# Kernel tuning notes

Hardware: AMD Instinct MI355X
Metric: run time of the kernel (lower is better)

## Reference

```python
import jax, jax.numpy as jnp
import numpy as np

HEADS = 8
DIM_HEAD = 64
WINDOW = 128
PERSIST = 4
EPS = 1.1920929e-07  # torch nn.RMSNorm default eps = finfo(fp32).eps


def _rope_freqs(n, d, dtype):
    inv_freq = 1.0 / (10000.0 ** (jnp.arange(0, d, 2, dtype=jnp.float32) / d))
    freqs = jnp.arange(n, dtype=jnp.float32)[:, None] * inv_freq[None, :]  # [n, d/2]
    freqs = jnp.repeat(freqs, 2, axis=-1)  # interleaved repeat -> [n, d]
    return jnp.cos(freqs).astype(dtype), jnp.sin(freqs).astype(dtype)


def _rotate_half(x):
    # interleaved pairs (x0,x1),(x2,x3)... -> (-x1,x0),(-x3,x2)...
    x = x.reshape(*x.shape[:-1], -1, 2)
    x1, x2 = x[..., 0], x[..., 1]
    return jnp.stack((-x2, x1), axis=-1).reshape(*x.shape[:-2], -1)


def setup_inputs() -> dict:
    key = jax.random.key(0)
    k1, k2, k3 = jax.random.split(key, 3)
    B, N, D = 1, 4096, 1024
    dim_inner = HEADS * DIM_HEAD  # 512
    return {
        "seq": jax.random.normal(k1, (B, N, D), dtype=jnp.float32),
        "g": jnp.ones((D,), dtype=jnp.float32),
        "w_qkv": jax.random.normal(k2, (D, 3 * dim_inner), dtype=jnp.float32) * 0.02,
        "w_out": jax.random.normal(k3, (dim_inner, D), dtype=jnp.float32) * 0.02,
    }


def reference(seq, g, w_qkv, w_out):
    B, N, D = seq.shape
    H, Dh = HEADS, DIM_HEAD

    # RMSNorm
    x = seq * jax.lax.rsqrt(jnp.mean(seq * seq, axis=-1, keepdims=True) + EPS) * g

    # QKV projection -> [B, H, N, Dh]
    qkv = x @ w_qkv
    q, k, v = jnp.split(qkv, 3, axis=-1)
    to_heads = lambda t: t.reshape(B, N, H, Dh).transpose(0, 2, 1, 3)
    q, k, v = map(to_heads, (q, k, v))

    # rotary embeddings (same positions for q and k)
    cos, sin = _rope_freqs(N, Dh, q.dtype)
    q = q * cos + _rotate_half(q) * sin
    k = k * cos + _rotate_half(k) * sin

    # causal & (persist | sliding-window) mask
    idx = jnp.arange(N)
    dist = idx[:, None] - idx[None, :]
    mask = (dist >= 0) & ((idx[None, :] < PERSIST) | (dist <= WINDOW))  # [N, N]

    scale = Dh ** -0.5
    scores = jnp.einsum("bhid,bhjd->bhij", q, k) * scale
    neg = -jnp.finfo(scores.dtype).max
    scores = jnp.where(mask[None, None], scores, neg)
    attn = jax.nn.softmax(scores, axis=-1)
    out = jnp.einsum("bhij,bhjd->bhid", attn, v)

    out = out.transpose(0, 2, 1, 3).reshape(B, N, H * Dh)
    return out @ w_out
```

## Files before the change

### kernel.cpp

```cpp
#include <hip/hip_runtime.h>
#include <hip/hip_bf16.h>
#include <math.h>

#define SEQ    4096
#define DMODEL 1024
#define NHEADS 8
#define DH     64
#define DINNER 512
#define NQKV   1536
#define WINDOW 128
#define PERSIST 4
#define EPS 1.1920929e-07f

typedef unsigned short u16;
typedef unsigned int   u32;
typedef __bf16  bf16_8 __attribute__((ext_vector_type(8)));
typedef float   f32x4  __attribute__((ext_vector_type(4)));

__device__ __forceinline__ u16 f2b(float f) {
    union { float f; u32 i; } v; v.f = f;
    u32 i = v.i;
    u32 r = (i + 0x7fffu + ((i >> 16) & 1u)) >> 16;
    return (u16)r;
}

#define GLD16(gp, lp) __builtin_amdgcn_global_load_lds( \
    (const __attribute__((address_space(1))) void*)(gp), \
    (__attribute__((address_space(3))) void*)(lp), 16, 0, 0)

__device__ __forceinline__ void transpose_tile(const float* __restrict__ src,
                                               u16* __restrict__ dst,
                                               int K, int N, int bn, int bk,
                                               u16 (*t)[65], int tid) {
    int r = tid >> 4, c4 = (tid & 15) * 4;
    #pragma unroll
    for (int it = 0; it < 4; it++) {
        int row = r + it * 16;
        float4 v = *(const float4*)(src + (size_t)(bk + row) * N + bn + c4);
        t[row][c4 + 0] = f2b(v.x);
        t[row][c4 + 1] = f2b(v.y);
        t[row][c4 + 2] = f2b(v.z);
        t[row][c4 + 3] = f2b(v.w);
    }
    __syncthreads();
    #pragma unroll
    for (int it = 0; it < 4; it++) {
        int n = r + it * 16;
        u16* d = dst + (size_t)(bn + n) * K + bk + c4;
        uint2 o;
        o.x = (u32)t[c4 + 0][n] | ((u32)t[c4 + 1][n] << 16);
        o.y = (u32)t[c4 + 2][n] | ((u32)t[c4 + 3][n] << 16);
        *(uint2*)d = o;
    }
}

__global__ __launch_bounds__(256) void prep_kernel(const float* __restrict__ wqkv,
                                                   const float* __restrict__ wout,
                                                   const float* __restrict__ seq,
                                                   const float* __restrict__ g,
                                                   u16* __restrict__ wqkv_bt,
                                                   u16* __restrict__ wout_bt,
                                                   u16* __restrict__ x) {
    __shared__ u16 t[64][65];
    __shared__ float wsum[4];
    int b = blockIdx.x, tid = threadIdx.x;
    if (b < 384) {
        transpose_tile(wqkv, wqkv_bt, DMODEL, NQKV, (b % 24) * 64, (b / 24) * 64, t, tid);
    } else if (b < 512) {
        int bb = b - 384;
        transpose_tile(wout, wout_bt, DINNER, DMODEL, (bb % 16) * 64, (bb / 16) * 64, t, tid);
    } else {
        int row = b - 512;
        float4 v = *(const float4*)(seq + (size_t)row * DMODEL + tid * 4);
        float ss = v.x*v.x + v.y*v.y + v.z*v.z + v.w*v.w;
        #pragma unroll
        for (int o = 32; o > 0; o >>= 1) ss += __shfl_xor(ss, o);
        if ((tid & 63) == 0) wsum[tid >> 6] = ss;
        __syncthreads();
        float tot = wsum[0] + wsum[1] + wsum[2] + wsum[3];
        float rstd = rsqrtf(tot * (1.0f / DMODEL) + EPS);
        float4 gv = *(const float4*)(g + tid * 4);
        uint2 o;
        o.x = (u32)f2b(v.x * rstd * gv.x) | ((u32)f2b(v.y * rstd * gv.y) << 16);
        o.y = (u32)f2b(v.z * rstd * gv.z) | ((u32)f2b(v.w * rstd * gv.w) << 16);
        *(uint2*)(x + (size_t)row * DMODEL + tid * 4) = o;
    }
}

__global__ __launch_bounds__(512, 2) void gemm_qkv(const u16* __restrict__ A,
                                                   const u16* __restrict__ Bt,
                                                   u16* __restrict__ C0,
                                                   u16* __restrict__ C1,
                                                   u16* __restrict__ C2) {
    __shared__ u16 As[2][128 * 64];
    __shared__ u16 Bs[2][192 * 64];
    int lin = blockIdx.y * 8 + blockIdx.x;
    int swz = (lin & 7) * 32 + (lin >> 3);
    int bx = swz & 7, by = swz >> 3;
    int tid = threadIdx.x;
    int lane = tid & 63, wave = tid >> 6;
    int m16 = lane & 15, quad = lane >> 4;
    int rw0 = (wave & 1) * 64, cw0 = (wave >> 1) * 48;

    f32x4 acc[4][3];
    #pragma unroll
    for (int mt = 0; mt < 4; mt++)
        #pragma unroll
        for (int nt = 0; nt < 3; nt++) acc[mt][nt] = (f32x4){0.f, 0.f, 0.f, 0.f};

    int lrow = lane & 7, lkc = lane >> 3;
    const u16* Ag = A  + (size_t)(by * 128 + lrow) * DMODEL + lkc * 8;
    const u16* Bg = Bt + (size_t)(bx * 192 + lrow) * DMODEL + lkc * 8;

    auto stage_tile = [&](int tt, int bb) {
        int k0 = tt * 64;
        #pragma unroll
        for (int r = 0; r < 2; r++) {
            int gg = wave * 2 + r;
            GLD16(Ag + (size_t)(gg * 8) * DMODEL + k0, &As[bb][0] + gg * 512);
        }
        #pragma unroll
        for (int r = 0; r < 3; r++) {
            int gg = wave * 3 + r;
            GLD16(Bg + (size_t)(gg * 8) * DMODEL + k0, &Bs[bb][0] + gg * 512);
        }
    };
    auto compute_tile = [&](int bb) {
        #pragma unroll
        for (int kk = 0; kk < 2; kk++) {
            int kc = kk * 4 + quad;
            bf16_8 afr[4], bfr[3];
            #pragma unroll
            for (int mt = 0; mt < 4; mt++) {
                int row = rw0 + mt * 16 + m16;
                afr[mt] = *(const bf16_8*)(&As[bb][0] + (row >> 3) * 512 + kc * 64 + (row & 7) * 8);
            }
            #pragma unroll
            for (int nt = 0; nt < 3; nt++) {
                int col = cw0 + nt * 16 + m16;
                bfr[nt] = *(const bf16_8*)(&Bs[bb][0] + (col >> 3) * 512 + kc * 64 + (col & 7) * 8);
            }
            #pragma unroll
            for (int mt = 0; mt < 4; mt++)
                #pragma unroll
                for (int nt = 0; nt < 3; nt++)
                    acc[mt][nt] = __builtin_amdgcn_mfma_f32_16x16x32_bf16(afr[mt], bfr[nt], acc[mt][nt], 0, 0, 0);
        }
    };

    stage_tile(0, 0);
    #pragma unroll 1
    for (int t = 0; t < 15; t++) {
        int cur = t & 1;
        stage_tile(t + 1, cur ^ 1);
        asm volatile("s_waitcnt vmcnt(5)" ::: "memory");
        __builtin_amdgcn_s_barrier();
        __builtin_amdgcn_sched_barrier(0);
        compute_tile(cur);
        __builtin_amdgcn_s_barrier();
    }
    asm volatile("s_waitcnt vmcnt(0)" ::: "memory");
    __builtin_amdgcn_s_barrier();
    __builtin_amdgcn_sched_barrier(0);
    compute_tile(1);

    #pragma unroll
    for (int nt = 0; nt < 3; nt++) {
        int col = bx * 192 + cw0 + nt * 16 + m16;
        int tens = col >> 9, hh = (col >> 6) & 7, dh = col & 63;
        if (tens == 2) {
            #pragma unroll
            for (int mt = 0; mt < 4; mt++) {
                int nb = by * 128 + rw0 + mt * 16 + quad * 4;
                uint2 o;
                o.x = (u32)f2b(acc[mt][nt][0]) | ((u32)f2b(acc[mt][nt][1]) << 16);
                o.y = (u32)f2b(acc[mt][nt][2]) | ((u32)f2b(acc[mt][nt][3]) << 16);
                *(uint2*)(C2 + ((size_t)(hh * DH + dh)) * SEQ + nb) = o;
            }
        } else {
            int tt = (col & 63) >> 1;
            float inv = exp2f(-(float)(2 * tt) * (13.287712379549449f / 64.0f));
            bool odd = (col & 1);
            u16* dst = (tens == 0) ? C0 : C1;
            #pragma unroll
            for (int mt = 0; mt < 4; mt++) {
                #pragma unroll
                for (int r = 0; r < 4; r++) {
                    int row = by * 128 + rw0 + mt * 16 + quad * 4 + r;
                    float own = acc[mt][nt][r];
                    float part = __shfl_xor(own, 1);
                    float s, c;
                    __sincosf((float)row * inv, &s, &c);
                    float val = odd ? (own * c + part * s) : (own * c - part * s);
                    dst[((size_t)hh * SEQ + row) * DH + dh] = f2b(val);
                }
            }
        }
    }
}

__global__ __launch_bounds__(256, 2) void gemm_out(const u16* __restrict__ A,
                                                   const u16* __restrict__ Bt,
                                                   float* __restrict__ Cf) {
    constexpr int BN = 64, GPW = 2, NT = DINNER / 64;
    __shared__ u16 As[2][128 * 64];
    __shared__ u16 Bs[2][BN * 64];
    int bx = blockIdx.x, by = blockIdx.y, tid = threadIdx.x;
    int lane = tid & 63, wave = tid >> 6;
    int m16 = lane & 15, quad = lane >> 4;
    int rw0 = (wave & 1) * 64, cw0 = (wave >> 1) * 32;

    f32x4 acc[4][2];
    #pragma unroll
    for (int mt = 0; mt < 4; mt++)
        #pragma unroll
        for (int nt = 0; nt < 2; nt++) acc[mt][nt] = (f32x4){0.f, 0.f, 0.f, 0.f};

    int lrow = lane & 7, lkc = lane >> 3;
    const u16* Ag = A  + (size_t)(by * 128 + lrow) * DINNER + lkc * 8;
    const u16* Bg = Bt + (size_t)(bx * BN  + lrow) * DINNER + lkc * 8;

    auto stage_tile = [&](int tt, int bb) {
        int k0 = tt * 64;
        #pragma unroll
        for (int r = 0; r < 4; r++) {
            int gg = wave * 4 + r;
            GLD16(Ag + (size_t)(gg * 8) * DINNER + k0, &As[bb][0] + gg * 512);
        }
        #pragma unroll
        for (int r = 0; r < GPW; r++) {
            int gg = wave * GPW + r;
            GLD16(Bg + (size_t)(gg * 8) * DINNER + k0, &Bs[bb][0] + gg * 512);
        }
    };
    auto compute_tile = [&](int bb) {
        #pragma unroll
        for (int kk = 0; kk < 2; kk++) {
            int kc = kk * 4 + quad;
            bf16_8 afr[4], bfr[2];
            #pragma unroll
            for (int mt = 0; mt < 4; mt++) {
                int row = rw0 + mt * 16 + m16;
                afr[mt] = *(const bf16_8*)(&As[bb][0] + (row >> 3) * 512 + kc * 64 + (row & 7) * 8);
            }
            #pragma unroll
            for (int nt = 0; nt < 2; nt++) {
                int col = cw0 + nt * 16 + m16;
                bfr[nt] = *(const bf16_8*)(&Bs[bb][0] + (col >> 3) * 512 + kc * 64 + (col & 7) * 8);
            }
            #pragma unroll
            for (int mt = 0; mt < 4; mt++)
                #pragma unroll
                for (int nt = 0; nt < 2; nt++)
                    acc[mt][nt] = __builtin_amdgcn_mfma_f32_16x16x32_bf16(afr[mt], bfr[nt], acc[mt][nt], 0, 0, 0);
        }
    };

    stage_tile(0, 0);
    #pragma unroll 1
    for (int t = 0; t < NT - 1; t++) {
        int cur = t & 1;
        stage_tile(t + 1, cur ^ 1);
        asm volatile("s_waitcnt vmcnt(6)" ::: "memory");
        __builtin_amdgcn_s_barrier();
        __builtin_amdgcn_sched_barrier(0);
        compute_tile(cur);
        __builtin_amdgcn_s_barrier();
    }
    asm volatile("s_waitcnt vmcnt(0)" ::: "memory");
    __builtin_amdgcn_s_barrier();
    __builtin_amdgcn_sched_barrier(0);
    compute_tile((NT - 1) & 1);

    #pragma unroll
    for (int nt = 0; nt < 2; nt++) {
        int col = bx * BN + cw0 + nt * 16 + m16;
        #pragma unroll
        for (int mt = 0; mt < 4; mt++) {
            #pragma unroll
            for (int r = 0; r < 4; r++) {
                int row = by * 128 + rw0 + mt * 16 + quad * 4 + r;
                Cf[(size_t)row * DMODEL + col] = acc[mt][nt][r];
            }
        }
    }
}

#define AROWS 208
#define KLD   72
#define PLD   168
#define VLD   222

__global__ __launch_bounds__(256, 2) void attn_mfma(const u16* __restrict__ Q,
                                                    const u16* __restrict__ Kt,
                                                    const u16* __restrict__ Vg,
                                                    u16* __restrict__ O) {
    __shared__ __align__(16) char smem[29952 + 64 * VLD * 2];
    u16* Ks = (u16*)smem;
    u16* Ps = (u16*)smem;
    u16* Vt = (u16*)(smem + 29952);
    int i0 = blockIdx.x * 64, h = blockIdx.y;
    int tid = threadIdx.x, wave = tid >> 6, lane = tid & 63;
    int m16 = lane & 15, quad = lane >> 4;
    int smin = (i0 > WINDOW) ? i0 - WINDOW : 0;

    for (int idx = tid; idx < AROWS * 8; idx += 256) {
        int row = idx >> 3, c = idx & 7;
        int j = (row < 16) ? row : (smin + row - 16);
        *(bf16_8*)(Ks + row * KLD + c * 8) =
            *(const bf16_8*)(Kt + ((size_t)h * SEQ + j) * DH + c * 8);
    }
    for (int idx = tid; idx < 64 * 26; idx += 256) {
        int d = idx / 26, c = idx - d * 26;
        int t0 = c * 8;
        int n0 = (c < 2) ? t0 : (smin + t0 - 16);
        *(bf16_8*)(Vt + d * VLD + t0) =
            *(const bf16_8*)(Vg + ((size_t)(h * DH + d)) * SEQ + n0);
    }

    int iw0 = i0 + wave * 16;
    int iq = iw0 + m16;
    const u16* qrow = Q + ((size_t)h * SEQ + iq) * DH;
    bf16_8 qa = *(const bf16_8*)(qrow + quad * 8);
    bf16_8 qb = *(const bf16_8*)(qrow + 32 + quad * 8);
    __syncthreads();

    int start_w = (iw0 > WINDOW) ? iw0 - WINDOW : 0;
    int Dw = start_w - smin;
    int tlast = 31 + iw0 - start_w;
    int nch = (tlast >> 4) + 1;
    int nk32 = (tlast >> 5) + 1;

    f32x4 S[10];
    __builtin_amdgcn_s_setprio(1);
    #pragma unroll
    for (int c = 0; c < 10; c++) {
        if (c < nch) {
            int t = c * 16 + m16;
            int row = (c == 0) ? t : (t + Dw);
            const u16* kp = Ks + row * KLD;
            bf16_8 kb0 = *(const bf16_8*)(kp + quad * 8);
            bf16_8 kb1 = *(const bf16_8*)(kp + 32 + quad * 8);
            f32x4 s = (f32x4){0.f, 0.f, 0.f, 0.f};
            s = __builtin_amdgcn_mfma_f32_16x16x32_bf16(qa, kb0, s, 0, 0, 0);
            s = __builtin_amdgcn_mfma_f32_16x16x32_bf16(qb, kb1, s, 0, 0, 0);
            S[c] = s;
        }
    }
    __builtin_amdgcn_s_setprio(0);
    __syncthreads();

    float mrow[4] = {-1e30f, -1e30f, -1e30f, -1e30f};
    #pragma unroll
    for (int c = 0; c < 10; c++) {
        if (c < nch) {
            int t = c * 16 + m16;
            int j = (c == 0) ? t : (start_w + t - 16);
            #pragma unroll
            for (int r = 0; r < 4; r++) {
                int i = iw0 + quad * 4 + r;
                bool valid = (c == 0) ? (j < PERSIST && j < start_w)
                                      : (j <= i && (i - j <= WINDOW || j < PERSIST));
                float sv = valid ? S[c][r] * 0.125f : -1e30f;
                S[c][r] = sv;
                mrow[r] = fmaxf(mrow[r], sv);
            }
        }
    }
    #pragma unroll
    for (int r = 0; r < 4; r++) {
        #pragma unroll
        for (int o = 1; o < 16; o <<= 1) mrow[r] = fmaxf(mrow[r], __shfl_xor(mrow[r], o));
    }
    float srow[4] = {0.f, 0.f, 0.f, 0.f};
    #pragma unroll
    for (int c = 0; c < 10; c++) {
        if (c < nch) {
            #pragma unroll
            for (int r = 0; r < 4; r++) {
                float p = __expf(S[c][r] - mrow[r]);
                S[c][r] = p;
                srow[r] += p;
            }
        }
    }
    #pragma unroll
    for (int r = 0; r < 4; r++) {
        #pragma unroll
        for (int o = 1; o < 16; o <<= 1) srow[r] += __shfl_xor(srow[r], o);
    }

    u16* pw = Ps + wave * 16 * PLD;
    #pragma unroll
    for (int c = 0; c < 10; c++) {
        #pragma unroll
        for (int r = 0; r < 4; r++) {
            u16 val = (c < nch) ? f2b(S[c][r]) : (u16)0;
            pw[(quad * 4 + r) * PLD + c * 16 + m16] = val;
        }
    }

    f32x4 oacc[4];
    #pragma unroll
    for (int nt = 0; nt < 4; nt++) oacc[nt] = (f32x4){0.f, 0.f, 0.f, 0.f};
    __builtin_amdgcn_s_setprio(1);
    #pragma unroll
    for (int c2 = 0; c2 < 5; c2++) {
        if (c2 < nk32) {
            bf16_8 af = *(const bf16_8*)(pw + m16 * PLD + c2 * 32 + quad * 8);
            int kbase = c2 * 32 + quad * 8;
            int rowb = (kbase < 16) ? kbase : (kbase + Dw);
            #pragma unroll
            for (int nt = 0; nt < 4; nt++) {
                int d = nt * 16 + m16;
                bf16_8 bv = *(const bf16_8*)(Vt + d * VLD + rowb);
                oacc[nt] = __builtin_amdgcn_mfma_f32_16x16x32_bf16(af, bv, oacc[nt], 0, 0, 0);
            }
        }
    }
    __builtin_amdgcn_s_setprio(0);

    float rinv[4];
    #pragma unroll
    for (int r = 0; r < 4; r++) rinv[r] = 1.0f / srow[r];
    #pragma unroll
    for (int nt = 0; nt < 4; nt++) {
        #pragma unroll
        for (int r = 0; r < 4; r++) {
            int i = iw0 + quad * 4 + r;
            O[(size_t)i * DINNER + h * DH + nt * 16 + m16] = f2b(oacc[nt][r] * rinv[r]);
        }
    }
}

extern "C" void kernel_launch(void* const* d_in, const int* in_sizes, int n_in,
                              void* d_out, int out_size, void* d_ws, size_t ws_size,
                              hipStream_t stream) {
    const float* seq  = (const float*)d_in[0];
    const float* g    = (const float*)d_in[1];
    const float* wqkv = (const float*)d_in[2];
    const float* wout = (const float*)d_in[3];
    float* out = (float*)d_out;

    char* ws = (char*)d_ws;
    u16* x       = (u16*)(ws);
    u16* q       = (u16*)(ws + 8ll  * 1024 * 1024);
    u16* k       = (u16*)(ws + 12ll * 1024 * 1024);
    u16* v       = (u16*)(ws + 16ll * 1024 * 1024);
    u16* att     = (u16*)(ws + 20ll * 1024 * 1024);
    u16* wqkv_bt = (u16*)(ws + 24ll * 1024 * 1024);
    u16* wout_bt = (u16*)(ws + 27ll * 1024 * 1024);

    prep_kernel<<<4608, 256, 0, stream>>>(wqkv, wout, seq, g, wqkv_bt, wout_bt, x);

    dim3 gq(NQKV / 192, SEQ / 128);
    gemm_qkv<<<gq, 512, 0, stream>>>(x, wqkv_bt, q, k, v);

    dim3 g2(SEQ / 64, NHEADS);
    attn_mfma<<<g2, 256, 0, stream>>>(q, k, v, att);

    dim3 g3(DMODEL / 64, SEQ / 128);
    gemm_out<<<g3, 256, 0, stream>>>(att, wout_bt, out);
}
```

Before: 146.9 us.

## Pad global row strides for GEMM operands and drop QKV block swizzle

Row strides of the normalized activations, transposed weights, and attention output are padded (1024→1032, 512→520 elements) so strided global loads do not map onto the same memory channels or cache sets. The QKV GEMM drops its block-index swizzle in favour of plain grid order, and its launch bound is raised to 4 blocks per CU. Workspace offsets are shifted to fit the padded buffers. Dropping the swizzle may reduce L2 reuse, and the higher occupancy hint may constrain registers.

```diff
diff --git a/kernel.cpp b/kernel.cpp
--- a/kernel.cpp
+++ b/kernel.cpp
@@ -12,6 +12,9 @@
 #define PERSIST 4
 #define EPS 1.1920929e-07f
 
+#define XLD  1032
+#define ALD  520
+
 typedef unsigned short u16;
 typedef unsigned int   u32;
 typedef __bf16  bf16_8 __attribute__((ext_vector_type(8)));
@@ -30,7 +33,7 @@
 
 __device__ __forceinline__ void transpose_tile(const float* __restrict__ src,
                                                u16* __restrict__ dst,
-                                               int K, int N, int bn, int bk,
+                                               int DLD, int N, int bn, int bk,
                                                u16 (*t)[65], int tid) {
     int r = tid >> 4, c4 = (tid & 15) * 4;
     #pragma unroll
@@ -46,7 +49,7 @@
     #pragma unroll
     for (int it = 0; it < 4; it++) {
         int n = r + it * 16;
-        u16* d = dst + (size_t)(bn + n) * K + bk + c4;
+        u16* d = dst + (size_t)(bn + n) * DLD + bk + c4;
         uint2 o;
         o.x = (u32)t[c4 + 0][n] | ((u32)t[c4 + 1][n] << 16);
         o.y = (u32)t[c4 + 2][n] | ((u32)t[c4 + 3][n] << 16);
@@ -65,10 +68,10 @@
     __shared__ float wsum[4];
     int b = blockIdx.x, tid = threadIdx.x;
     if (b < 384) {
-        transpose_tile(wqkv, wqkv_bt, DMODEL, NQKV, (b % 24) * 64, (b / 24) * 64, t, tid);
+        transpose_tile(wqkv, wqkv_bt, XLD, NQKV, (b % 24) * 64, (b / 24) * 64, t, tid);
     } else if (b < 512) {
         int bb = b - 384;
-        transpose_tile(wout, wout_bt, DINNER, DMODEL, (bb % 16) * 64, (bb / 16) * 64, t, tid);
+        transpose_tile(wout, wout_bt, ALD, DMODEL, (bb % 16) * 64, (bb / 16) * 64, t, tid);
     } else {
         int row = b - 512;
         float4 v = *(const float4*)(seq + (size_t)row * DMODEL + tid * 4);
@@ -83,21 +86,18 @@
         uint2 o;
         o.x = (u32)f2b(v.x * rstd * gv.x) | ((u32)f2b(v.y * rstd * gv.y) << 16);
         o.y = (u32)f2b(v.z * rstd * gv.z) | ((u32)f2b(v.w * rstd * gv.w) << 16);
-        *(uint2*)(x + (size_t)row * DMODEL + tid * 4) = o;
-    }
-}
-
-__global__ __launch_bounds__(512, 2) void gemm_qkv(const u16* __restrict__ A,
+        *(uint2*)(x + (size_t)row * XLD + tid * 4) = o;
+    }
+}
+
+__global__ __launch_bounds__(512, 4) void gemm_qkv(const u16* __restrict__ A,
                                                    const u16* __restrict__ Bt,
                                                    u16* __restrict__ C0,
                                                    u16* __restrict__ C1,
                                                    u16* __restrict__ C2) {
     __shared__ u16 As[2][128 * 64];
     __shared__ u16 Bs[2][192 * 64];
-    int lin = blockIdx.y * 8 + blockIdx.x;
-    int swz = (lin & 7) * 32 + (lin >> 3);
-    int bx = swz & 7, by = swz >> 3;
-    int tid = threadIdx.x;
+    int bx = blockIdx.x, by = blockIdx.y, tid = threadIdx.x;
     int lane = tid & 63, wave = tid >> 6;
     int m16 = lane & 15, quad = lane >> 4;
     int rw0 = (wave & 1) * 64, cw0 = (wave >> 1) * 48;
@@ -109,20 +109,20 @@
         for (int nt = 0; nt < 3; nt++) acc[mt][nt] = (f32x4){0.f, 0.f, 0.f, 0.f};
 
     int lrow = lane & 7, lkc = lane >> 3;
-    const u16* Ag = A  + (size_t)(by * 128 + lrow) * DMODEL + lkc * 8;
-    const u16* Bg = Bt + (size_t)(bx * 192 + lrow) * DMODEL + lkc * 8;
+    const u16* Ag = A  + (size_t)(by * 128 + lrow) * XLD + lkc * 8;
+    const u16* Bg = Bt + (size_t)(bx * 192 + lrow) * XLD + lkc * 8;
 
     auto stage_tile = [&](int tt, int bb) {
         int k0 = tt * 64;
         #pragma unroll
         for (int r = 0; r < 2; r++) {
             int gg = wave * 2 + r;
-            GLD16(Ag + (size_t)(gg * 8) * DMODEL + k0, &As[bb][0] + gg * 512);
+            GLD16(Ag + (size_t)(gg * 8) * XLD + k0, &As[bb][0] + gg * 512);
         }
         #pragma unroll
         for (int r = 0; r < 3; r++) {
             int gg = wave * 3 + r;
-            GLD16(Bg + (size_t)(gg * 8) * DMODEL + k0, &Bs[bb][0] + gg * 512);
+            GLD16(Bg + (size_t)(gg * 8) * XLD + k0, &Bs[bb][0] + gg * 512);
         }
     };
     auto compute_tile = [&](int bb) {
@@ -217,20 +217,20 @@
         for (int nt = 0; nt < 2; nt++) acc[mt][nt] = (f32x4){0.f, 0.f, 0.f, 0.f};
 
     int lrow = lane & 7, lkc = lane >> 3;
-    const u16* Ag = A  + (size_t)(by * 128 + lrow) * DINNER + lkc * 8;
-    const u16* Bg = Bt + (size_t)(bx * BN  + lrow) * DINNER + lkc * 8;
+    const u16* Ag = A  + (size_t)(by * 128 + lrow) * ALD + lkc * 8;
+    const u16* Bg = Bt + (size_t)(bx * BN  + lrow) * ALD + lkc * 8;
 
     auto stage_tile = [&](int tt, int bb) {
         int k0 = tt * 64;
         #pragma unroll
         for (int r = 0; r < 4; r++) {
             int gg = wave * 4 + r;
-            GLD16(Ag + (size_t)(gg * 8) * DINNER + k0, &As[bb][0] + gg * 512);
+            GLD16(Ag + (size_t)(gg * 8) * ALD + k0, &As[bb][0] + gg * 512);
         }
         #pragma unroll
         for (int r = 0; r < GPW; r++) {
             int gg = wave * GPW + r;
-            GLD16(Bg + (size_t)(gg * 8) * DINNER + k0, &Bs[bb][0] + gg * 512);
+            GLD16(Bg + (size_t)(gg * 8) * ALD + k0, &Bs[bb][0] + gg * 512);
         }
     };
     auto compute_tile = [&](int bb) {
@@ -287,7 +287,7 @@
 }
 
 #define AROWS 208
-#define KLD   72
+#define KLD2  72
 #define PLD   168
 #define VLD   222
 
@@ -307,7 +307,7 @@
     for (int idx = tid; idx < AROWS * 8; idx += 256) {
         int row = idx >> 3, c = idx & 7;
         int j = (row < 16) ? row : (smin + row - 16);
-        *(bf16_8*)(Ks + row * KLD + c * 8) =
+        *(bf16_8*)(Ks + row * KLD2 + c * 8) =
             *(const bf16_8*)(Kt + ((size_t)h * SEQ + j) * DH + c * 8);
     }
     for (int idx = tid; idx < 64 * 26; idx += 256) {
@@ -338,7 +338,7 @@
         if (c < nch) {
             int t = c * 16 + m16;
             int row = (c == 0) ? t : (t + Dw);
-            const u16* kp = Ks + row * KLD;
+            const u16* kp = Ks + row * KLD2;
             bf16_8 kb0 = *(const bf16_8*)(kp + quad * 8);
             bf16_8 kb1 = *(const bf16_8*)(kp + 32 + quad * 8);
             f32x4 s = (f32x4){0.f, 0.f, 0.f, 0.f};
@@ -428,7 +428,7 @@
         #pragma unroll
         for (int r = 0; r < 4; r++) {
             int i = iw0 + quad * 4 + r;
-            O[(size_t)i * DINNER + h * DH + nt * 16 + m16] = f2b(oacc[nt][r] * rinv[r]);
+            O[(size_t)i * ALD + h * DH + nt * 16 + m16] = f2b(oacc[nt][r] * rinv[r]);
         }
     }
 }
@@ -444,17 +444,17 @@
 
     char* ws = (char*)d_ws;
     u16* x       = (u16*)(ws);
-    u16* q       = (u16*)(ws + 8ll  * 1024 * 1024);
-    u16* k       = (u16*)(ws + 12ll * 1024 * 1024);
-    u16* v       = (u16*)(ws + 16ll * 1024 * 1024);
-    u16* att     = (u16*)(ws + 20ll * 1024 * 1024);
-    u16* wqkv_bt = (u16*)(ws + 24ll * 1024 * 1024);
-    u16* wout_bt = (u16*)(ws + 27ll * 1024 * 1024);
+    u16* q       = (u16*)(ws + 9ll  * 1024 * 1024);
+    u16* k       = (u16*)(ws + 13ll * 1024 * 1024);
+    u16* v       = (u16*)(ws + 17ll * 1024 * 1024);
+    u16* att     = (u16*)(ws + 21ll * 1024 * 1024);
+    u16* wqkv_bt = (u16*)(ws + 26ll * 1024 * 1024);
+    u16* wout_bt = (u16*)(ws + 30ll * 1024 * 1024);
 
     prep_kernel<<<4608, 256, 0, stream>>>(wqkv, wout, seq, g, wqkv_bt, wout_bt, x);
 
-    dim3 gq(NQKV / 192, SEQ / 128);
-    gemm_qkv<<<gq, 512, 0, stream>>>(x, wqkv_bt, q, k, v);
+    dim3 g1(NQKV / 192, SEQ / 128);
+    gemm_qkv<<<g1, 512, 0, stream>>>(x, wqkv_bt, q, k, v);
 
     dim3 g2(SEQ / 64, NHEADS);
     attn_mfma<<<g2, 256, 0, stream>>>(q, k, v, att);
```

Result: faster. 137.8 us (-6.2%).
